# Optimization experiments

Measured on AMD Instinct MI355X. Metric: run time of the kernel, lower is better.

The kernel has to match this reference:

```python
import jax, jax.numpy as jnp
import numpy as np

LATENT = 128
HIDDEN = 512
N_STEPS = 50
BATCH = 8192


def _linear_init(k, fan_in, fan_out):
    kw, kb = jax.random.split(k)
    lim = 1.0 / np.sqrt(fan_in)
    W = jax.random.uniform(kw, (fan_in, fan_out), minval=-lim, maxval=lim, dtype=jnp.float32)
    b = jax.random.uniform(kb, (fan_out,), minval=-lim, maxval=lim, dtype=jnp.float32)
    return W, b


def setup_inputs() -> dict:
    key = jax.random.key(0)
    ks = jax.random.split(key, 6)
    in_dim = 2 * LATENT + 2  # x + condition + t_emb + target_emb
    W1, b1 = _linear_init(ks[0], in_dim, HIDDEN)
    W2, b2 = _linear_init(ks[1], HIDDEN, HIDDEN)
    W3, b3 = _linear_init(ks[2], HIDDEN, HIDDEN)
    W4, b4 = _linear_init(ks[3], HIDDEN, LATENT)
    condition = jax.random.normal(ks[4], (BATCH, LATENT), dtype=jnp.float32)
    x_init = jax.random.normal(ks[5], (BATCH, LATENT), dtype=jnp.float32)
    return dict(condition=condition, x_init=x_init,
                W1=W1, b1=b1, W2=W2, b2=b2, W3=W3, b3=b3, W4=W4, b4=b4,
                target_survival=1)


def reference(condition, x_init, W1, b1, W2, b2, W3, b3, W4, b4, target_survival):
    n_steps = N_STEPS
    betas = jnp.linspace(1e-4, 0.02, n_steps).astype(x_init.dtype)
    alphas = 1.0 - betas
    alphas_cumprod = jnp.cumprod(alphas)
    batch = condition.shape[0]
    # target = zeros if target_survival else ones (static python scalar)
    target = jnp.full((batch, 1), 0.0 if target_survival else 1.0, dtype=x_init.dtype)
    noise_key = jax.random.key(42)

    def step(x, t):
        t_emb = jnp.full((batch, 1), 1.0, x.dtype) * (t.astype(x.dtype) / n_steps)
        inp = jnp.concatenate([x, condition, t_emb, target], axis=-1)  # [B, 2L+2]
        h = jax.nn.gelu(inp @ W1 + b1, approximate=False)
        h = jax.nn.gelu(h @ W2 + b2, approximate=False)
        h = jax.nn.gelu(h @ W3 + b3, approximate=False)
        noise_pred = h @ W4 + b4  # [B, L]
        noise = jax.random.normal(jax.random.fold_in(noise_key, t), x.shape, x.dtype)
        noise = jnp.where(t > 0, noise, jnp.zeros_like(noise))  # no noise at t=0
        beta_t = betas[t]
        x = (x - beta_t / jnp.sqrt(1.0 - alphas_cumprod[t]) * noise_pred) / jnp.sqrt(alphas[t])
        x = x + jnp.sqrt(beta_t) * noise
        return x, None

    ts = jnp.arange(n_steps - 1, -1, -1)  # reversed(range(n_steps))
    x_final, _ = jax.lax.scan(step, x_init, ts)
    return x_final
```

## Files before the change

kernel.cpp:

```cpp
#include <hip/hip_runtime.h>
#include <stdint.h>
#include <stddef.h>


typedef __bf16 bf16;
typedef __bf16 bf16x4 __attribute__((ext_vector_type(4)));
typedef __bf16 bf16x8 __attribute__((ext_vector_type(8)));
typedef float  floatx4 __attribute__((ext_vector_type(4)));

#define NSTEPS    50
#define WG_ROWS   32
#define XB_STRIDE 136
#define H_STRIDE  520

__device__ __forceinline__ uint32_t rotl32(uint32_t x, int r) {
  return (x << r) | (x >> (32 - r));
}

__device__ __forceinline__ void threefry2x32(uint32_t k0, uint32_t k1,
                                             uint32_t x0, uint32_t x1,
                                             uint32_t& o0, uint32_t& o1) {
  uint32_t k2 = k0 ^ k1 ^ 0x1BD11BDAu;
  x0 += k0; x1 += k1;
#define TF_R(R) { x0 += x1; x1 = rotl32(x1, R); x1 ^= x0; }
  TF_R(13) TF_R(15) TF_R(26) TF_R(6)
  x0 += k1; x1 += k2 + 1u;
  TF_R(17) TF_R(29) TF_R(16) TF_R(24)
  x0 += k2; x1 += k0 + 2u;
  TF_R(13) TF_R(15) TF_R(26) TF_R(6)
  x0 += k0; x1 += k1 + 3u;
  TF_R(17) TF_R(29) TF_R(16) TF_R(24)
  x0 += k1; x1 += k2 + 4u;
  TF_R(13) TF_R(15) TF_R(26) TF_R(6)
  x0 += k2; x1 += k0 + 5u;
#undef TF_R
  o0 = x0; o1 = x1;
}

__device__ __forceinline__ float erfinv_xla_bl(float x) {
  float w = -0.6931471805599453f * __builtin_amdgcn_logf(fmaf(-x, x, 1.0f));
  float wa = w - 2.5f;
  float pa = 2.81022636e-08f;
  pa = fmaf(pa, wa, 3.43273939e-07f);
  pa = fmaf(pa, wa, -3.5233877e-06f);
  pa = fmaf(pa, wa, -4.39150654e-06f);
  pa = fmaf(pa, wa, 0.00021858087f);
  pa = fmaf(pa, wa, -0.00125372503f);
  pa = fmaf(pa, wa, -0.00417768164f);
  pa = fmaf(pa, wa, 0.246640727f);
  pa = fmaf(pa, wa, 1.50140941f);
  float wb = __builtin_amdgcn_sqrtf(w) - 3.0f;
  float pb = -0.000200214257f;
  pb = fmaf(pb, wb, 0.000100950558f);
  pb = fmaf(pb, wb, 0.00134934322f);
  pb = fmaf(pb, wb, -0.00367342844f);
  pb = fmaf(pb, wb, 0.00573950773f);
  pb = fmaf(pb, wb, -0.0076224613f);
  pb = fmaf(pb, wb, 0.00943887047f);
  pb = fmaf(pb, wb, 1.00167406f);
  pb = fmaf(pb, wb, 2.83297682f);
  float p = (w < 5.0f) ? pa : pb;
  return p * x;
}

__device__ __forceinline__ float gelu_fast(float x) {
  float z  = x * 0.7071067811865475f;
  float az = fabsf(z);
  float t  = __builtin_amdgcn_rcpf(fmaf(0.3275911f, az, 1.0f));
  float p  = fmaf(1.061405429f, t, -1.453152027f);
  p = fmaf(p, t, 1.421413741f);
  p = fmaf(p, t, -0.284496736f);
  p = fmaf(p, t, 0.254829592f);
  p *= t;
  float e  = __builtin_amdgcn_exp2f(az * az * -1.4426950408889634f);
  float er = fmaf(-p, e, 1.0f);
  er = copysignf(er, z);
  return 0.5f * x * (1.0f + er);
}

#define MFMA16(a, b, c) __builtin_amdgcn_mfma_f32_16x16x32_bf16((a), (b), (c), 0, 0, 0)

template<int KSTEPS, int BSTRIDE, int UNROLL>
__device__ __forceinline__ void gemm2t(const bf16* __restrict__ h_lds,
                                       const bf16* __restrict__ A_pk,
                                       int lane, floatx4 (&acc)[2][2]) {
  const int nrow = lane & 15, q = lane >> 4;
  const bf16* b0 = h_lds + nrow * BSTRIDE + q * 8;
  const bf16* a0 = A_pk + lane * 8;
#pragma unroll UNROLL
  for (int ks = 0; ks < KSTEPS; ++ks) {
    bf16x8 bf0 = *(const bf16x8*)(b0 + ks * 32);
    bf16x8 bf1 = *(const bf16x8*)(b0 + 16 * BSTRIDE + ks * 32);
    bf16x8 aA  = *(const bf16x8*)(a0 + ks * 512);
    bf16x8 aB  = *(const bf16x8*)(a0 + (KSTEPS + ks) * 512);
    acc[0][0] = MFMA16(aA, bf0, acc[0][0]);
    acc[0][1] = MFMA16(aA, bf1, acc[0][1]);
    acc[1][0] = MFMA16(aB, bf0, acc[1][0]);
    acc[1][1] = MFMA16(aB, bf1, acc[1][1]);
  }
}

__device__ __forceinline__ void gemm_l4(const bf16* __restrict__ h_lds,
                                        const bf16* __restrict__ A_pk,
                                        int lane, floatx4 (&acc4)[2]) {
  const int nrow = lane & 15, q = lane >> 4;
  const bf16* b0 = h_lds + nrow * H_STRIDE + q * 8;
  const bf16* a0 = A_pk + lane * 8;
#pragma unroll 4
  for (int ks = 0; ks < 16; ++ks) {
    bf16x8 bf0 = *(const bf16x8*)(b0 + ks * 32);
    bf16x8 bf1 = *(const bf16x8*)(b0 + 16 * H_STRIDE + ks * 32);
    bf16x8 af  = *(const bf16x8*)(a0 + ks * 512);
    acc4[0] = MFMA16(af, bf0, acc4[0]);
    acc4[1] = MFMA16(af, bf1, acc4[1]);
  }
}

__global__ void diff_prep(const float* __restrict__ W1, const float* __restrict__ b1,
                          const float* __restrict__ W2, const float* __restrict__ W3,
                          const float* __restrict__ W4, const int* __restrict__ tsurv,
                          bf16* __restrict__ w1p, bf16* __restrict__ w1cp,
                          bf16* __restrict__ w2p, bf16* __restrict__ w3p,
                          bf16* __restrict__ w4p,
                          float* __restrict__ eb1, uint32_t* __restrict__ fk,
                          float* __restrict__ cst) {
  const int tid = blockIdx.x * blockDim.x + threadIdx.x;
  const int nth = gridDim.x * blockDim.x;
  for (int i = tid; i < 512 * 128; i += nth) {
    int j = i & 7, lane = (i >> 3) & 63, ks = (i >> 9) & 3, ntg = i >> 11;
    int n = ntg * 16 + (lane & 15);
    int k = ks * 32 + (lane >> 4) * 8 + j;
    w1p[i]  = (bf16)W1[k * 512 + n];
    w1cp[i] = (bf16)W1[(128 + k) * 512 + n];
  }
  for (int i = tid; i < 512 * 512; i += nth) {
    int j = i & 7, lane = (i >> 3) & 63, ks = (i >> 9) & 15, ntg = i >> 13;
    int n = ntg * 16 + (lane & 15);
    int k = ks * 32 + (lane >> 4) * 8 + j;
    w2p[i] = (bf16)W2[k * 512 + n];
    w3p[i] = (bf16)W3[k * 512 + n];
  }
  for (int i = tid; i < 128 * 512; i += nth) {
    int j = i & 7, lane = (i >> 3) & 63, ks = (i >> 9) & 15, ntg = i >> 13;
    int n = ntg * 16 + (lane & 15);
    int k = ks * 32 + (lane >> 4) * 8 + j;
    w4p[i] = (bf16)W4[k * 128 + n];
  }
  const float tgt = (tsurv[0] != 0) ? 0.0f : 1.0f;
  for (int i = tid; i < NSTEPS * 512; i += nth) {
    int t = i >> 9, n = i & 511;
    eb1[i] = b1[n] + ((float)t / 50.0f) * W1[256 * 512 + n] + tgt * W1[257 * 512 + n];
  }
  if (tid == 0) {
    float ac = 1.0f;
    for (int t = 0; t < NSTEPS; ++t) {
      float beta  = 1e-4f + (0.02f - 1e-4f) * ((float)t / 49.0f);
      float alpha = 1.0f - beta;
      ac *= alpha;
      cst[t]            = beta / sqrtf(1.0f - ac);
      cst[NSTEPS + t]   = 1.0f / sqrtf(alpha);
      cst[2*NSTEPS + t] = sqrtf(beta);
      uint32_t o0, o1;
      threefry2x32(0u, 42u, 0u, (uint32_t)t, o0, o1);
      fk[t] = o0; fk[NSTEPS + t] = o1;
    }
  }
}

__global__ __launch_bounds__(512, 2) void diff_main(
    const float* __restrict__ cond, const float* __restrict__ xinit,
    const bf16* __restrict__ w1p, const bf16* __restrict__ w1cp,
    const bf16* __restrict__ w2p, const bf16* __restrict__ w3p,
    const bf16* __restrict__ w4p,
    const float* __restrict__ eb1, const float* __restrict__ b2,
    const float* __restrict__ b3, const float* __restrict__ b4,
    const uint32_t* __restrict__ fk, const float* __restrict__ cst,
    float* __restrict__ out) {
  __shared__ bf16 xb[WG_ROWS * XB_STRIDE];
  __shared__ bf16 hbA[WG_ROWS * H_STRIDE];
  __shared__ bf16 hbB[WG_ROWS * H_STRIDE];

  const int tid  = threadIdx.x;
  const int wave = tid >> 6;
  const int lane = tid & 63;
  const int nrow = lane & 15, q = lane >> 4;
  const int r0   = blockIdx.x * WG_ROWS;
  const int qc   = q * 4;
  const int xc0  = wave * 16 + qc;

  const bf16* w4base = w4p + wave * 16 * 512;

  {
    const int row = tid >> 4;
    const int c0  = (tid & 15) * 8;
    float4 a  = *(const float4*)(xinit + (size_t)(r0 + row) * 128 + c0);
    float4 a2 = *(const float4*)(xinit + (size_t)(r0 + row) * 128 + c0 + 4);
    float4 c  = *(const float4*)(cond  + (size_t)(r0 + row) * 128 + c0);
    float4 c2 = *(const float4*)(cond  + (size_t)(r0 + row) * 128 + c0 + 4);
    bf16x8 xs, cs;
    xs[0] = (bf16)a.x;  xs[1] = (bf16)a.y;  xs[2] = (bf16)a.z;  xs[3] = (bf16)a.w;
    xs[4] = (bf16)a2.x; xs[5] = (bf16)a2.y; xs[6] = (bf16)a2.z; xs[7] = (bf16)a2.w;
    cs[0] = (bf16)c.x;  cs[1] = (bf16)c.y;  cs[2] = (bf16)c.z;  cs[3] = (bf16)c.w;
    cs[4] = (bf16)c2.x; cs[5] = (bf16)c2.y; cs[6] = (bf16)c2.z; cs[7] = (bf16)c2.w;
    *(bf16x8*)(xb  + row * XB_STRIDE + c0) = xs;
    *(bf16x8*)(hbA + row * H_STRIDE  + c0) = cs;
  }
  float4 xregA = *(const float4*)(xinit + (size_t)(r0 + nrow)      * 128 + xc0);
  float4 xregB = *(const float4*)(xinit + (size_t)(r0 + nrow + 16) * 128 + xc0);
  __syncthreads();

  floatx4 cpr[2][2][2] = {};
#pragma unroll
  for (int p = 0; p < 2; ++p)
    gemm2t<4, H_STRIDE, 4>(hbA, w1cp + ((p * 8 + wave) * 2) * 4 * 512, lane, cpr[p]);
  __syncthreads();

  for (int t = NSTEPS - 1; t >= 0; --t) {
    {
      const float* ebt = eb1 + t * 512;
#pragma unroll
      for (int p = 0; p < 2; ++p) {
        floatx4 acc[2][2] = {};
        gemm2t<4, XB_STRIDE, 4>(xb, w1p + ((p * 8 + wave) * 2) * 4 * 512, lane, acc);
        const int pc0 = (p * 8 + wave) * 32;
#pragma unroll
        for (int mt = 0; mt < 2; ++mt) {
          const int col = pc0 + mt * 16 + qc;
          float4 bb = *(const float4*)(ebt + col);
#pragma unroll
          for (int nt = 0; nt < 2; ++nt) {
            bf16x4 g;
#pragma unroll
            for (int r = 0; r < 4; ++r)
              g[r] = (bf16)gelu_fast(acc[mt][nt][r] + cpr[p][mt][nt][r] + ((const float*)&bb)[r]);
            *(bf16x4*)(hbA + (nt * 16 + nrow) * H_STRIDE + col) = g;
          }
        }
      }
    }
    __syncthreads();

    {
#pragma unroll
      for (int p = 0; p < 2; ++p) {
        floatx4 acc[2][2] = {};
        gemm2t<16, H_STRIDE, 4>(hbA, w2p + ((p * 8 + wave) * 2) * 16 * 512, lane, acc);
        const int pc0 = (p * 8 + wave) * 32;
#pragma unroll
        for (int mt = 0; mt < 2; ++mt) {
          const int col = pc0 + mt * 16 + qc;
          float4 bb = *(const float4*)(b2 + col);
#pragma unroll
          for (int nt = 0; nt < 2; ++nt) {
            bf16x4 g;
#pragma unroll
            for (int r = 0; r < 4; ++r)
              g[r] = (bf16)gelu_fast(acc[mt][nt][r] + ((const float*)&bb)[r]);
            *(bf16x4*)(hbB + (nt * 16 + nrow) * H_STRIDE + col) = g;
          }
        }
      }
    }
    __syncthreads();

    {
#pragma unroll
      for (int p = 0; p < 2; ++p) {
        floatx4 acc[2][2] = {};
        gemm2t<16, H_STRIDE, 4>(hbB, w3p + ((p * 8 + wave) * 2) * 16 * 512, lane, acc);
        const int pc0 = (p * 8 + wave) * 32;
#pragma unroll
        for (int mt = 0; mt < 2; ++mt) {
          const int col = pc0 + mt * 16 + qc;
          float4 bb = *(const float4*)(b3 + col);
#pragma unroll
          for (int nt = 0; nt < 2; ++nt) {
            bf16x4 g;
#pragma unroll
            for (int r = 0; r < 4; ++r)
              g[r] = (bf16)gelu_fast(acc[mt][nt][r] + ((const float*)&bb)[r]);
            *(bf16x4*)(hbA + (nt * 16 + nrow) * H_STRIDE + col) = g;
          }
        }
      }
    }
    __syncthreads();

    {
      floatx4 acc4[2] = {};
      gemm_l4(hbA, w4base, lane, acc4);
      const float c1 = cst[t], c2 = cst[NSTEPS + t], c3 = cst[2 * NSTEPS + t];
      const uint32_t fk0 = fk[t], fk1 = fk[NSTEPS + t];
      const float zscale = (t > 0) ? 1.4142135381698608f : 0.0f;
      float4 bb = *(const float4*)(b4 + xc0);
      const uint32_t gbaseA = (uint32_t)(r0 + nrow) * 128u + (uint32_t)xc0;
      const uint32_t gbaseB = (uint32_t)(r0 + nrow + 16) * 128u + (uint32_t)xc0;

      float z[8];
#pragma unroll
      for (int r = 0; r < 8; ++r) {
        const uint32_t gi = (r < 4) ? (gbaseA + (uint32_t)r) : (gbaseB + (uint32_t)(r - 4));
        uint32_t o0, o1;
        threefry2x32(fk0, fk1, 0u, gi, o0, o1);
        uint32_t bits = o0 ^ o1;
        float f01 = __uint_as_float((bits >> 9) | 0x3F800000u) - 1.0f;
        float u = fmaxf(-0.99999994f, fmaf(f01, 2.0f, -0.99999994f));
        z[r] = zscale * erfinv_xla_bl(u);
      }

      bf16x4 xpkA, xpkB;
#pragma unroll
      for (int r = 0; r < 4; ++r) {
        float npA = acc4[0][r] + ((const float*)&bb)[r];
        float xnA = (((float*)&xregA)[r] - c1 * npA) * c2 + c3 * z[r];
        ((float*)&xregA)[r] = xnA;
        xpkA[r] = (bf16)xnA;
        float npB = acc4[1][r] + ((const float*)&bb)[r];
        float xnB = (((float*)&xregB)[r] - c1 * npB) * c2 + c3 * z[r + 4];
        ((float*)&xregB)[r] = xnB;
        xpkB[r] = (bf16)xnB;
      }
      *(bf16x4*)(xb + nrow * XB_STRIDE + xc0)        = xpkA;
      *(bf16x4*)(xb + (nrow + 16) * XB_STRIDE + xc0) = xpkB;
    }
    __syncthreads();
  }

  *(float4*)(out + (size_t)(r0 + nrow)      * 128 + xc0) = xregA;
  *(float4*)(out + (size_t)(r0 + nrow + 16) * 128 + xc0) = xregB;
}

extern "C" void kernel_launch(void* const* d_in, const int* in_sizes, int n_in,
                              void* d_out, int out_size, void* d_ws, size_t ws_size,
                              hipStream_t stream) {
  const float* cond  = (const float*)d_in[0];
  const float* xinit = (const float*)d_in[1];
  const float* W1 = (const float*)d_in[2];
  const float* b1 = (const float*)d_in[3];
  const float* W2 = (const float*)d_in[4];
  const float* b2 = (const float*)d_in[5];
  const float* W3 = (const float*)d_in[6];
  const float* b3 = (const float*)d_in[7];
  const float* W4 = (const float*)d_in[8];
  const float* b4 = (const float*)d_in[9];
  const int* tsurv = (const int*)d_in[10];

  char* ws = (char*)d_ws;
  bf16* w1p  = (bf16*)(ws + 0);
  bf16* w1cp = (bf16*)(ws + 131072);
  bf16* w2p  = (bf16*)(ws + 262144);
  bf16* w3p  = (bf16*)(ws + 786432);
  bf16* w4p  = (bf16*)(ws + 1310720);
  float* eb1 = (float*)(ws + 1441792);
  uint32_t* fkp = (uint32_t*)(ws + 1544192);
  float* cstp = (float*)(ws + 1544704);

  diff_prep<<<1024, 256, 0, stream>>>(W1, b1, W2, W3, W4, tsurv,
                                      w1p, w1cp, w2p, w3p, w4p, eb1, fkp, cstp);
  diff_main<<<256, 512, 0, stream>>>(cond, xinit, w1p, w1cp, w2p, w3p, w4p,
                                     eb1, b2, b3, b4, fkp, cstp, (float*)d_out);
}
```

Baseline: 1.028 ms.

## Keep W1 x-weights in registers and prefetch next-layer weight heads across barriers

The W1 x-part weights are loaded once into registers and reused every step instead of being reloaded from global memory. The first k-steps of each following layer's weights (W2, W3, W4, then W2 again) are prefetched into registers during the previous layer's work, so their global latency overlaps the barrier. To make room for the extra registers, occupancy is lowered from two workgroups per CU to one, which risks less latency hiding across workgroups.

```diff
diff --git a/kernel.cpp b/kernel.cpp
--- a/kernel.cpp
+++ b/kernel.cpp
@@ -100,20 +100,80 @@
   }
 }
 
-__device__ __forceinline__ void gemm_l4(const bf16* __restrict__ h_lds,
-                                        const bf16* __restrict__ A_pk,
-                                        int lane, floatx4 (&acc4)[2]) {
+template<int KSTEPS, int BSTRIDE>
+__device__ __forceinline__ void gemm2t_pre(const bf16* __restrict__ h_lds,
+                                           const bf16* __restrict__ A_pk,
+                                           const bf16x8 (&pf)[4],
+                                           int lane, floatx4 (&acc)[2][2]) {
+  const int nrow = lane & 15, q = lane >> 4;
+  const bf16* b0 = h_lds + nrow * BSTRIDE + q * 8;
+  {
+    bf16x8 bf0 = *(const bf16x8*)(b0);
+    bf16x8 bf1 = *(const bf16x8*)(b0 + 16 * BSTRIDE);
+    acc[0][0] = MFMA16(pf[0], bf0, acc[0][0]);
+    acc[0][1] = MFMA16(pf[0], bf1, acc[0][1]);
+    acc[1][0] = MFMA16(pf[2], bf0, acc[1][0]);
+    acc[1][1] = MFMA16(pf[2], bf1, acc[1][1]);
+    bf0 = *(const bf16x8*)(b0 + 32);
+    bf1 = *(const bf16x8*)(b0 + 16 * BSTRIDE + 32);
+    acc[0][0] = MFMA16(pf[1], bf0, acc[0][0]);
+    acc[0][1] = MFMA16(pf[1], bf1, acc[0][1]);
+    acc[1][0] = MFMA16(pf[3], bf0, acc[1][0]);
+    acc[1][1] = MFMA16(pf[3], bf1, acc[1][1]);
+  }
+  const bf16* a0 = A_pk + lane * 8;
+#pragma unroll 4
+  for (int ks = 2; ks < KSTEPS; ++ks) {
+    bf16x8 bf0 = *(const bf16x8*)(b0 + ks * 32);
+    bf16x8 bf1 = *(const bf16x8*)(b0 + 16 * BSTRIDE + ks * 32);
+    bf16x8 aA  = *(const bf16x8*)(a0 + ks * 512);
+    bf16x8 aB  = *(const bf16x8*)(a0 + (KSTEPS + ks) * 512);
+    acc[0][0] = MFMA16(aA, bf0, acc[0][0]);
+    acc[0][1] = MFMA16(aA, bf1, acc[0][1]);
+    acc[1][0] = MFMA16(aB, bf0, acc[1][0]);
+    acc[1][1] = MFMA16(aB, bf1, acc[1][1]);
+  }
+}
+
+__device__ __forceinline__ void gemm_l4_pre(const bf16* __restrict__ h_lds,
+                                            const bf16* __restrict__ A_pk,
+                                            const bf16x8 (&pf)[4],
+                                            int lane, floatx4 (&acc4)[2]) {
   const int nrow = lane & 15, q = lane >> 4;
   const bf16* b0 = h_lds + nrow * H_STRIDE + q * 8;
+#pragma unroll
+  for (int ks = 0; ks < 4; ++ks) {
+    bf16x8 bf0 = *(const bf16x8*)(b0 + ks * 32);
+    bf16x8 bf1 = *(const bf16x8*)(b0 + 16 * H_STRIDE + ks * 32);
+    acc4[0] = MFMA16(pf[ks], bf0, acc4[0]);
+    acc4[1] = MFMA16(pf[ks], bf1, acc4[1]);
+  }
   const bf16* a0 = A_pk + lane * 8;
 #pragma unroll 4
-  for (int ks = 0; ks < 16; ++ks) {
+  for (int ks = 4; ks < 16; ++ks) {
     bf16x8 bf0 = *(const bf16x8*)(b0 + ks * 32);
     bf16x8 bf1 = *(const bf16x8*)(b0 + 16 * H_STRIDE + ks * 32);
     bf16x8 af  = *(const bf16x8*)(a0 + ks * 512);
     acc4[0] = MFMA16(af, bf0, acc4[0]);
     acc4[1] = MFMA16(af, bf1, acc4[1]);
   }
+}
+
+__device__ __forceinline__ void pf_head16(const bf16* __restrict__ base,
+                                          int lane, bf16x8 (&pf)[4]) {
+  const bf16* a0 = base + lane * 8;
+  pf[0] = *(const bf16x8*)(a0);
+  pf[1] = *(const bf16x8*)(a0 + 512);
+  pf[2] = *(const bf16x8*)(a0 + 16 * 512);
+  pf[3] = *(const bf16x8*)(a0 + 17 * 512);
+}
+
+__device__ __forceinline__ void pf_head4(const bf16* __restrict__ base,
+                                         int lane, bf16x8 (&pf)[4]) {
+  const bf16* a0 = base + lane * 8;
+#pragma unroll
+  for (int ks = 0; ks < 4; ++ks)
+    pf[ks] = *(const bf16x8*)(a0 + ks * 512);
 }
 
 __global__ void diff_prep(const float* __restrict__ W1, const float* __restrict__ b1,
@@ -167,7 +227,7 @@
   }
 }
 
-__global__ __launch_bounds__(512, 2) void diff_main(
+__global__ __launch_bounds__(512, 1) void diff_main(
     const float* __restrict__ cond, const float* __restrict__ xinit,
     const bf16* __restrict__ w1p, const bf16* __restrict__ w1cp,
     const bf16* __restrict__ w2p, const bf16* __restrict__ w3p,
@@ -188,6 +248,10 @@
   const int qc   = q * 4;
   const int xc0  = wave * 16 + qc;
 
+  const bf16* w2p0 = w2p + (wave * 2) * 16 * 512;
+  const bf16* w2p1 = w2p + ((8 + wave) * 2) * 16 * 512;
+  const bf16* w3p0 = w3p + (wave * 2) * 16 * 512;
+  const bf16* w3p1 = w3p + ((8 + wave) * 2) * 16 * 512;
   const bf16* w4base = w4p + wave * 16 * 512;
 
   {
@@ -213,15 +277,37 @@
 #pragma unroll
   for (int p = 0; p < 2; ++p)
     gemm2t<4, H_STRIDE, 4>(hbA, w1cp + ((p * 8 + wave) * 2) * 4 * 512, lane, cpr[p]);
+
+  bf16x8 w1r[2][2][4];
+#pragma unroll
+  for (int p = 0; p < 2; ++p)
+#pragma unroll
+    for (int mt = 0; mt < 2; ++mt)
+#pragma unroll
+      for (int ks = 0; ks < 4; ++ks)
+        w1r[p][mt][ks] = *(const bf16x8*)(
+            w1p + ((((p * 8 + wave) * 2 + mt) * 4 + ks) * 64 + lane) * 8);
+
+  bf16x8 pf[4];
+  pf_head16(w2p0, lane, pf);
   __syncthreads();
 
   for (int t = NSTEPS - 1; t >= 0; --t) {
     {
       const float* ebt = eb1 + t * 512;
+      const bf16* b0 = xb + nrow * XB_STRIDE + q * 8;
 #pragma unroll
       for (int p = 0; p < 2; ++p) {
         floatx4 acc[2][2] = {};
-        gemm2t<4, XB_STRIDE, 4>(xb, w1p + ((p * 8 + wave) * 2) * 4 * 512, lane, acc);
+#pragma unroll
+        for (int ks = 0; ks < 4; ++ks) {
+          bf16x8 bf0 = *(const bf16x8*)(b0 + ks * 32);
+          bf16x8 bf1 = *(const bf16x8*)(b0 + 16 * XB_STRIDE + ks * 32);
+          acc[0][0] = MFMA16(w1r[p][0][ks], bf0, acc[0][0]);
+          acc[0][1] = MFMA16(w1r[p][0][ks], bf1, acc[0][1]);
+          acc[1][0] = MFMA16(w1r[p][1][ks], bf0, acc[1][0]);
+          acc[1][1] = MFMA16(w1r[p][1][ks], bf1, acc[1][1]);
+        }
         const int pc0 = (p * 8 + wave) * 32;
 #pragma unroll
         for (int mt = 0; mt < 2; ++mt) {
@@ -241,11 +327,10 @@
     __syncthreads();
 
     {
-#pragma unroll
-      for (int p = 0; p < 2; ++p) {
+      {
         floatx4 acc[2][2] = {};
-        gemm2t<16, H_STRIDE, 4>(hbA, w2p + ((p * 8 + wave) * 2) * 16 * 512, lane, acc);
-        const int pc0 = (p * 8 + wave) * 32;
+        gemm2t_pre<16, H_STRIDE>(hbA, w2p0, pf, lane, acc);
+        const int pc0 = wave * 32;
 #pragma unroll
         for (int mt = 0; mt < 2; ++mt) {
           const int col = pc0 + mt * 16 + qc;
@@ -260,15 +345,33 @@
           }
         }
       }
+      {
+        floatx4 acc[2][2] = {};
+        gemm2t<16, H_STRIDE, 4>(hbA, w2p1, lane, acc);
+        pf_head16(w3p0, lane, pf);
+        const int pc0 = (8 + wave) * 32;
+#pragma unroll
+        for (int mt = 0; mt < 2; ++mt) {
+          const int col = pc0 + mt * 16 + qc;
+          float4 bb = *(const float4*)(b2 + col);
+#pragma unroll
+          for (int nt = 0; nt < 2; ++nt) {
+            bf16x4 g;
+#pragma unroll
+            for (int r = 0; r < 4; ++r)
+              g[r] = (bf16)gelu_fast(acc[mt][nt][r] + ((const float*)&bb)[r]);
+            *(bf16x4*)(hbB + (nt * 16 + nrow) * H_STRIDE + col) = g;
+          }
+        }
+      }
     }
     __syncthreads();
 
     {
-#pragma unroll
-      for (int p = 0; p < 2; ++p) {
+      {
         floatx4 acc[2][2] = {};
-        gemm2t<16, H_STRIDE, 4>(hbB, w3p + ((p * 8 + wave) * 2) * 16 * 512, lane, acc);
-        const int pc0 = (p * 8 + wave) * 32;
+        gemm2t_pre<16, H_STRIDE>(hbB, w3p0, pf, lane, acc);
+        const int pc0 = wave * 32;
 #pragma unroll
         for (int mt = 0; mt < 2; ++mt) {
           const int col = pc0 + mt * 16 + qc;
@@ -283,12 +386,33 @@
           }
         }
       }
+      {
+        floatx4 acc[2][2] = {};
+        gemm2t<16, H_STRIDE, 4>(hbB, w3p1, lane, acc);
+        pf_head4(w4base, lane, pf);
+        const int pc0 = (8 + wave) * 32;
+#pragma unroll
+        for (int mt = 0; mt < 2; ++mt) {
+          const int col = pc0 + mt * 16 + qc;
+          float4 bb = *(const float4*)(b3 + col);
+#pragma unroll
+          for (int nt = 0; nt < 2; ++nt) {
+            bf16x4 g;
+#pragma unroll
+            for (int r = 0; r < 4; ++r)
+              g[r] = (bf16)gelu_fast(acc[mt][nt][r] + ((const float*)&bb)[r]);
+            *(bf16x4*)(hbA + (nt * 16 + nrow) * H_STRIDE + col) = g;
+          }
+        }
+      }
     }
     __syncthreads();
 
     {
       floatx4 acc4[2] = {};
-      gemm_l4(hbA, w4base, lane, acc4);
+      gemm_l4_pre(hbA, w4base, pf, lane, acc4);
+      pf_head16(w2p0, lane, pf);
+
       const float c1 = cst[t], c2 = cst[NSTEPS + t], c3 = cst[2 * NSTEPS + t];
       const uint32_t fk0 = fk[t], fk1 = fk[NSTEPS + t];
       const float zscale = (t > 0) ? 1.4142135381698608f : 0.0f;
```

Result: slower. 2.494 ms (+142.6%).
